# Optimization experiments

Measured on AMD Instinct MI355X. Metric: run time of the kernel, lower is better.

## Reference

```python
import jax, jax.numpy as jnp
import numpy as np

TAU = 2.0
V_TH = 1.0


def setup_inputs() -> dict:
    key = jax.random.key(0)
    k1, k2, k3 = jax.random.split(key, 3)
    T, B, N = 128, 64, 1024
    x = jax.random.normal(k1, (T, B, N), dtype=jnp.float32)
    # nn.Linear(hidden, hidden, bias=False) weights: [out, in]
    scale = 1.0 / np.sqrt(N)
    W1 = jax.random.uniform(k2, (N, N), dtype=jnp.float32, minval=-scale, maxval=scale)
    W2 = jax.random.uniform(k3, (N, N), dtype=jnp.float32, minval=-scale, maxval=scale)
    return {"x": x, "W1": W1, "W2": W2}


def _lif_scan(h_seq):
    # h_seq: [T, B, N]; LIF recurrence with tau=2, v_th=1, reset v = h*(1-s)
    def step(v, x_t):
        h = v + (x_t - v) / TAU
        s = (h >= V_TH).astype(h.dtype)
        return h * (1.0 - s), s

    v0 = jnp.zeros(h_seq.shape[1:], dtype=h_seq.dtype)
    _, spikes = jax.lax.scan(step, v0, h_seq)
    return spikes  # [T, B, N]


def reference(x, W1, W2):
    # fc1: y = x @ W1^T (torch Linear convention)
    h = jnp.einsum('tbn,mn->tbm', x, W1)
    spike = _lif_scan(h)
    return jnp.einsum('tbn,mn->tbm', spike, W2)
```

## Files before the change

### kernel.cpp

```cpp
#include <hip/hip_runtime.h>
#include <hip/hip_bf16.h>
#include <stdint.h>


#define TT 128
#define BB 64
#define NN 1024
#define MROWS (TT * BB)
#define SROW  (BB * NN)
#define MiB   ((size_t)1048576)

typedef _Float16 h8  __attribute__((ext_vector_type(8)));
typedef _Float16 h4v __attribute__((ext_vector_type(4)));
typedef float    f4  __attribute__((ext_vector_type(4)));
typedef float v2f __attribute__((ext_vector_type(2)));

#if __has_builtin(__builtin_elementwise_fma)
#define V2FMA(a, b, c) __builtin_elementwise_fma((a), (b), (c))
#else
static __device__ __forceinline__ v2f v2fma_(v2f a, v2f b, v2f c) {
    v2f r; r[0] = fmaf(a[0], b[0], c[0]); r[1] = fmaf(a[1], b[1], c[1]); return r;
}
#define V2FMA(a, b, c) v2fma_((a), (b), (c))
#endif

#define GL2LDS(g, l) __builtin_amdgcn_global_load_lds(                         \
    (const __attribute__((address_space(1))) void*)(const void*)(g),           \
    (__attribute__((address_space(3))) void*)(void*)(l), 16, 0, 0)

__global__ __launch_bounds__(256) void split2_f16(const float* __restrict__ src,
                                                  _Float16* __restrict__ d0,
                                                  _Float16* __restrict__ d1, int n4) {
    const int i = blockIdx.x * 256 + threadIdx.x;
    if (i >= n4) return;
    const float4 v = reinterpret_cast<const float4*>(src)[i];
    const float f[4] = {v.x, v.y, v.z, v.w};
    h4v a0, a1;
#pragma unroll
    for (int j = 0; j < 4; ++j) {
        const _Float16 c = (_Float16)f[j];
        a0[j] = c;
        a1[j] = (_Float16)((f[j] - (float)c) * 4096.0f);
    }
    reinterpret_cast<h4v*>(d0)[i] = a0;
    reinterpret_cast<h4v*>(d1)[i] = a1;
}

__global__ __launch_bounds__(256, 2) void gemm_split(const _Float16* __restrict__ A0,
                                                     const _Float16* __restrict__ A1,
                                                     const _Float16* __restrict__ B0,
                                                     const _Float16* __restrict__ B1,
                                                     float* __restrict__ C) {
    __shared__ _Float16 As[128 * 32];
    __shared__ _Float16 Bs[128 * 32];
    const int tid  = threadIdx.x;
    const int lane = tid & 63;
    const int wid  = tid >> 6;
    const int wr   = wid >> 1, wc = wid & 1;
    const int rowBase = blockIdx.y * 128;
    const int colBase = blockIdx.x * 128;

    const size_t aOff0 = (size_t)(rowBase + wid * 32 + (lane >> 2)) * NN + (lane & 3) * 8;
    const size_t aOff1 = aOff0 + (size_t)16 * NN;
    const size_t bOff0 = (size_t)(colBase + wid * 32 + (lane >> 2)) * NN + (lane & 3) * 8;
    const size_t bOff1 = bOff0 + (size_t)16 * NN;
    const int ldsW0 = (wid * 2 + 0) * 512;
    const int ldsW1 = (wid * 2 + 1) * 512;

    const int fA = (wr * 64 + (lane & 15)) * 32 + (lane >> 4) * 8;
    const int fB = (wc * 64 + (lane & 15)) * 32 + (lane >> 4) * 8;

    f4 acc0[4][4], acc1[4][4];
#pragma unroll
    for (int i = 0; i < 4; ++i)
#pragma unroll
        for (int j = 0; j < 4; ++j) { acc0[i][j] = (f4)0.0f; acc1[i][j] = (f4)0.0f; }

#define STAGE(AG, BG, K0)                                 \
    do {                                                  \
        GL2LDS((AG) + aOff0 + (K0), &As[ldsW0]);          \
        GL2LDS((AG) + aOff1 + (K0), &As[ldsW1]);          \
        GL2LDS((BG) + bOff0 + (K0), &Bs[ldsW0]);          \
        GL2LDS((BG) + bOff1 + (K0), &Bs[ldsW1]);          \
    } while (0)

#define PASS(AG, BG, ACC)                                                          \
    for (int k0 = 0; k0 < NN; k0 += 32) {                                          \
        STAGE(AG, BG, k0);                                                         \
        __syncthreads();                                                           \
        {                                                                          \
            h8 af0 = *(const h8*)&As[fA];                                          \
            h8 af1 = *(const h8*)&As[fA + 512];                                    \
            h8 af2 = *(const h8*)&As[fA + 1024];                                   \
            h8 af3 = *(const h8*)&As[fA + 1536];                                   \
            h8 bf0 = *(const h8*)&Bs[fB];                                          \
            h8 bf1 = *(const h8*)&Bs[fB + 512];                                    \
            h8 bf2 = *(const h8*)&Bs[fB + 1024];                                   \
            h8 bf3 = *(const h8*)&Bs[fB + 1536];                                   \
            ACC[0][0] = __builtin_amdgcn_mfma_f32_16x16x32_f16(af0, bf0, ACC[0][0], 0, 0, 0); \
            ACC[0][1] = __builtin_amdgcn_mfma_f32_16x16x32_f16(af0, bf1, ACC[0][1], 0, 0, 0); \
            ACC[0][2] = __builtin_amdgcn_mfma_f32_16x16x32_f16(af0, bf2, ACC[0][2], 0, 0, 0); \
            ACC[0][3] = __builtin_amdgcn_mfma_f32_16x16x32_f16(af0, bf3, ACC[0][3], 0, 0, 0); \
            ACC[1][0] = __builtin_amdgcn_mfma_f32_16x16x32_f16(af1, bf0, ACC[1][0], 0, 0, 0); \
            ACC[1][1] = __builtin_amdgcn_mfma_f32_16x16x32_f16(af1, bf1, ACC[1][1], 0, 0, 0); \
            ACC[1][2] = __builtin_amdgcn_mfma_f32_16x16x32_f16(af1, bf2, ACC[1][2], 0, 0, 0); \
            ACC[1][3] = __builtin_amdgcn_mfma_f32_16x16x32_f16(af1, bf3, ACC[1][3], 0, 0, 0); \
            ACC[2][0] = __builtin_amdgcn_mfma_f32_16x16x32_f16(af2, bf0, ACC[2][0], 0, 0, 0); \
            ACC[2][1] = __builtin_amdgcn_mfma_f32_16x16x32_f16(af2, bf1, ACC[2][1], 0, 0, 0); \
            ACC[2][2] = __builtin_amdgcn_mfma_f32_16x16x32_f16(af2, bf2, ACC[2][2], 0, 0, 0); \
            ACC[2][3] = __builtin_amdgcn_mfma_f32_16x16x32_f16(af2, bf3, ACC[2][3], 0, 0, 0); \
            ACC[3][0] = __builtin_amdgcn_mfma_f32_16x16x32_f16(af3, bf0, ACC[3][0], 0, 0, 0); \
            ACC[3][1] = __builtin_amdgcn_mfma_f32_16x16x32_f16(af3, bf1, ACC[3][1], 0, 0, 0); \
            ACC[3][2] = __builtin_amdgcn_mfma_f32_16x16x32_f16(af3, bf2, ACC[3][2], 0, 0, 0); \
            ACC[3][3] = __builtin_amdgcn_mfma_f32_16x16x32_f16(af3, bf3, ACC[3][3], 0, 0, 0); \
        }                                                                          \
        __syncthreads();                                                           \
    }

    PASS(A0, B0, acc0)
    PASS(A0, B1, acc1)
    PASS(A1, B0, acc1)
#undef PASS
#undef STAGE

    const int orow = rowBase + wr * 64 + (lane >> 4) * 4;
    const int ocol = colBase + wc * 64 + (lane & 15);
#pragma unroll
    for (int i = 0; i < 4; ++i)
#pragma unroll
        for (int j = 0; j < 4; ++j)
#pragma unroll
            for (int q = 0; q < 4; ++q)
                C[(size_t)(orow + i * 16 + q) * NN + ocol + j * 16] =
                    acc0[i][j][q] + acc1[i][j][q] * (1.0f / 4096.0f);
}

__global__ __launch_bounds__(256) void lif_scan(const float* __restrict__ H,
                                                unsigned long long* __restrict__ mask) {
    const int g = blockIdx.x * 256 + threadIdx.x;
    const int b = g >> 10;
    const int n = g & 1023;
    const int word = n >> 6;
    const bool lane0 = (threadIdx.x & 63) == 0;

    float v = 0.0f;
    float buf[8];
#pragma unroll
    for (int j = 0; j < 8; ++j) buf[j] = H[(size_t)j * SROW + g];

    for (int t0 = 0; t0 < TT; t0 += 8) {
        float nbuf[8];
        if (t0 + 8 < TT) {
#pragma unroll
            for (int j = 0; j < 8; ++j) nbuf[j] = H[(size_t)(t0 + 8 + j) * SROW + g];
        } else {
#pragma unroll
            for (int j = 0; j < 8; ++j) nbuf[j] = 0.f;
        }
#pragma unroll
        for (int j = 0; j < 8; ++j) {
            const float x = buf[j];
            const float h = v + (x - v) * 0.5f;
            const bool s = (h >= 1.0f);
            v = s ? 0.0f : h;
            const unsigned long long m = __ballot(s);
            if (lane0) mask[((size_t)(t0 + j) * BB + b) * 16 + word] = m;
        }
#pragma unroll
        for (int j = 0; j < 8; ++j) buf[j] = nbuf[j];
    }
}

__global__ __launch_bounds__(256) void transpose_nn(const float* __restrict__ in,
                                                    float* __restrict__ out) {
    __shared__ float tile[32][33];
    const int bx = blockIdx.x * 32, by = blockIdx.y * 32;
    {
        const int x = bx + threadIdx.x;
#pragma unroll
        for (int j = 0; j < 32; j += 8)
            tile[threadIdx.y + j][threadIdx.x] = in[(size_t)(by + threadIdx.y + j) * NN + x];
    }
    __syncthreads();
    {
        const int x = by + threadIdx.x;
#pragma unroll
        for (int j = 0; j < 32; j += 8)
            out[(size_t)(bx + threadIdx.y + j) * NN + x] = tile[threadIdx.x][threadIdx.y + j];
    }
}

__global__ __launch_bounds__(256) void spike_matmul(const unsigned long long* __restrict__ mask,
                                                    const float* __restrict__ W2T,
                                                    float* __restrict__ out) {
    __shared__ unsigned long long sw[16];
    const int r = blockIdx.x;
    const int tid = threadIdx.x;
    if (tid < 16) sw[tid] = mask[(size_t)r * 16 + tid];
    __syncthreads();

    float acc0 = 0.f, acc1 = 0.f, acc2 = 0.f, acc3 = 0.f;
#pragma unroll 1
    for (int w = 0; w < 16; ++w) {
        unsigned long long bits = sw[w];
        while (bits) {
            const int n = w * 64 + (__ffsll(bits) - 1);
            bits &= bits - 1;
            const float* __restrict__ row = W2T + (size_t)n * NN;
            acc0 += row[tid];
            acc1 += row[tid + 256];
            acc2 += row[tid + 512];
            acc3 += row[tid + 768];
        }
    }
    float* o = out + (size_t)r * NN;
    o[tid]       = acc0;
    o[tid + 256] = acc1;
    o[tid + 512] = acc2;
    o[tid + 768] = acc3;
}

#define BM 128
#define BN 64
#define BK 16
__global__ __launch_bounds__(256, 4) void gemm1_f32(const float* __restrict__ A,
                                                    const float* __restrict__ B,
                                                    float* __restrict__ C) {
    __shared__ float Asb[2][BK][132];
    __shared__ float Bsb[2][BK][68];
    const int tid = threadIdx.x;
    const int ty = tid >> 4;
    const int tx = tid & 15;
    const int rowBase = blockIdx.y * BM;
    const int colBase = blockIdx.x * BN;
    const int sr = tid >> 2;
    const int sk = (tid & 3) * 4;

    const float* Ap0 = A + (size_t)(rowBase + sr) * NN + sk;
    const float* Ap1 = Ap0 + (size_t)64 * NN;
    const float* Bp  = B + (size_t)(colBase + sr) * NN + sk;

    v2f acc[4][4];
#pragma unroll
    for (int i = 0; i < 4; ++i)
#pragma unroll
        for (int j = 0; j < 4; ++j) acc[i][j] = (v2f){0.f, 0.f};

    float4 ra0 = *(const float4*)Ap0;
    float4 ra1 = *(const float4*)Ap1;
    float4 rb  = *(const float4*)Bp;

#define STW(buf)                                                                       \
    do {                                                                               \
        Asb[buf][sk + 0][sr] = ra0.x; Asb[buf][sk + 1][sr] = ra0.y;                    \
        Asb[buf][sk + 2][sr] = ra0.z; Asb[buf][sk + 3][sr] = ra0.w;                    \
        Asb[buf][sk + 0][sr + 64] = ra1.x; Asb[buf][sk + 1][sr + 64] = ra1.y;          \
        Asb[buf][sk + 2][sr + 64] = ra1.z; Asb[buf][sk + 3][sr + 64] = ra1.w;          \
        Bsb[buf][sk + 0][sr] = rb.x;  Bsb[buf][sk + 1][sr] = rb.y;                     \
        Bsb[buf][sk + 2][sr] = rb.z;  Bsb[buf][sk + 3][sr] = rb.w;                     \
    } while (0)

    STW(0);
    __syncthreads();
    const int NT = NN / BK;
    for (int t = 0; t < NT; ++t) {
        const int cur = t & 1;
        if (t < NT - 1) {
            const int ko = (t + 1) * BK;
            ra0 = *(const float4*)(Ap0 + ko);
            ra1 = *(const float4*)(Ap1 + ko);
            rb  = *(const float4*)(Bp + ko);
        }
#pragma unroll
        for (int k = 0; k < BK; ++k) {
            const v2f* ap = (const v2f*)&Asb[cur][k][ty * 8];
            const float4 bf = *(const float4*)&Bsb[cur][k][tx * 4];
            const float bb[4] = {bf.x, bf.y, bf.z, bf.w};
            const v2f a0 = ap[0], a1 = ap[1], a2 = ap[2], a3 = ap[3];
#pragma unroll
            for (int j = 0; j < 4; ++j) {
                const v2f bd = {bb[j], bb[j]};
                acc[0][j] = V2FMA(a0, bd, acc[0][j]);
                acc[1][j] = V2FMA(a1, bd, acc[1][j]);
                acc[2][j] = V2FMA(a2, bd, acc[2][j]);
                acc[3][j] = V2FMA(a3, bd, acc[3][j]);
            }
        }
        if (t < NT - 1) STW(cur ^ 1);
        __syncthreads();
    }
#undef STW
    float* Cp = C + (size_t)(rowBase + ty * 8) * NN + colBase + tx * 4;
#pragma unroll
    for (int rp = 0; rp < 4; ++rp) {
        float4 lo = {acc[rp][0][0], acc[rp][1][0], acc[rp][2][0], acc[rp][3][0]};
        float4 hi = {acc[rp][0][1], acc[rp][1][1], acc[rp][2][1], acc[rp][3][1]};
        *(float4*)(Cp + (size_t)(2 * rp) * NN)     = lo;
        *(float4*)(Cp + (size_t)(2 * rp + 1) * NN) = hi;
    }
}

extern "C" void kernel_launch(void* const* d_in, const int* in_sizes, int n_in,
                              void* d_out, int out_size, void* d_ws, size_t ws_size,
                              hipStream_t stream) {
    const float* x  = (const float*)d_in[0];
    const float* W1 = (const float*)d_in[1];
    const float* W2 = (const float*)d_in[2];
    float* out = (float*)d_out;

    unsigned long long* mask = (unsigned long long*)d_ws;
    float* W2T = (float*)((char*)d_ws + 1 * MiB);

    if (ws_size >= 43 * MiB) {
        _Float16* A0 = (_Float16*)((char*)d_ws + 5 * MiB);
        _Float16* A1 = (_Float16*)((char*)d_ws + 22 * MiB);
        _Float16* B0 = (_Float16*)((char*)d_ws + 39 * MiB);
        _Float16* B1 = (_Float16*)((char*)d_ws + 41 * MiB);

        split2_f16<<<8192, 256, 0, stream>>>(x, A0, A1, MROWS * NN / 4);
        split2_f16<<<1024, 256, 0, stream>>>(W1, B0, B1, NN * NN / 4);
        transpose_nn<<<dim3(32, 32), dim3(32, 8), 0, stream>>>(W2, W2T);
        gemm_split<<<dim3(NN / 128, MROWS / 128), 256, 0, stream>>>(A0, A1, B0, B1, out);
    } else {
        transpose_nn<<<dim3(32, 32), dim3(32, 8), 0, stream>>>(W2, W2T);
        gemm1_f32<<<dim3(NN / BN, MROWS / BM), 256, 0, stream>>>(x, W1, out);
    }
    lif_scan<<<SROW / 256, 256, 0, stream>>>(out, mask);
    spike_matmul<<<MROWS, 256, 0, stream>>>(mask, W2T, out);
}
```

Before: 192.0 us.

## Double-buffer fused split GEMM, swizzle LDS, merge prep kernels, vectorize spike matmul

The three split-precision GEMM passes become a single K loop that loads all four fp16 operand tiles together, with a double-buffered LDS prefetch of the next K slice and XOR-swizzled LDS layout to cut bank conflicts. The two split kernels and the W2 transpose are merged into one prep launch to reduce launch overhead. The spike matmul now reads each W2T row as float4 vectors per thread instead of four strided scalars. LDS use per block quadruples (64 KiB), which may limit occupancy to fewer blocks per CU.

```diff
diff --git a/kernel.cpp b/kernel.cpp
--- a/kernel.cpp
+++ b/kernel.cpp
@@ -13,7 +13,7 @@
 typedef _Float16 h8  __attribute__((ext_vector_type(8)));
 typedef _Float16 h4v __attribute__((ext_vector_type(4)));
 typedef float    f4  __attribute__((ext_vector_type(4)));
-typedef float v2f __attribute__((ext_vector_type(2)));
+typedef float    v2f __attribute__((ext_vector_type(2)));
 
 #if __has_builtin(__builtin_elementwise_fma)
 #define V2FMA(a, b, c) __builtin_elementwise_fma((a), (b), (c))
@@ -28,22 +28,44 @@
     (const __attribute__((address_space(1))) void*)(const void*)(g),           \
     (__attribute__((address_space(3))) void*)(void*)(l), 16, 0, 0)
 
-__global__ __launch_bounds__(256) void split2_f16(const float* __restrict__ src,
-                                                  _Float16* __restrict__ d0,
-                                                  _Float16* __restrict__ d1, int n4) {
-    const int i = blockIdx.x * 256 + threadIdx.x;
-    if (i >= n4) return;
-    const float4 v = reinterpret_cast<const float4*>(src)[i];
-    const float f[4] = {v.x, v.y, v.z, v.w};
-    h4v a0, a1;
-#pragma unroll
-    for (int j = 0; j < 4; ++j) {
-        const _Float16 c = (_Float16)f[j];
-        a0[j] = c;
-        a1[j] = (_Float16)((f[j] - (float)c) * 4096.0f);
-    }
-    reinterpret_cast<h4v*>(d0)[i] = a0;
-    reinterpret_cast<h4v*>(d1)[i] = a1;
+__global__ __launch_bounds__(256) void prep(const float* __restrict__ x,
+                                            const float* __restrict__ W1,
+                                            const float* __restrict__ W2,
+                                            _Float16* __restrict__ A0, _Float16* __restrict__ A1,
+                                            _Float16* __restrict__ B0, _Float16* __restrict__ B1,
+                                            float* __restrict__ W2T) {
+    const int nb = blockIdx.x;
+    const int tid = threadIdx.x;
+    if (nb < 8192 + 1024) {
+        const bool isX = nb < 8192;
+        const float* src = isX ? x : W1;
+        _Float16* d0 = isX ? A0 : B0;
+        _Float16* d1 = isX ? A1 : B1;
+        const int i = (isX ? nb : nb - 8192) * 256 + tid;
+        const float4 v = reinterpret_cast<const float4*>(src)[i];
+        const float f[4] = {v.x, v.y, v.z, v.w};
+        h4v a0, a1;
+#pragma unroll
+        for (int j = 0; j < 4; ++j) {
+            const _Float16 c = (_Float16)f[j];
+            a0[j] = c;
+            a1[j] = (_Float16)((f[j] - (float)c) * 4096.0f);
+        }
+        reinterpret_cast<h4v*>(d0)[i] = a0;
+        reinterpret_cast<h4v*>(d1)[i] = a1;
+    } else {
+        __shared__ float tile[32][33];
+        const int tIdx = nb - 9216;
+        const int bx = (tIdx & 31) * 32, by = (tIdx >> 5) * 32;
+        const int tx = tid & 31, ty = tid >> 5;
+#pragma unroll
+        for (int j = 0; j < 32; j += 8)
+            tile[ty + j][tx] = W2[(size_t)(by + ty + j) * NN + bx + tx];
+        __syncthreads();
+#pragma unroll
+        for (int j = 0; j < 32; j += 8)
+            W2T[(size_t)(bx + ty + j) * NN + by + tx] = tile[tx][ty + j];
+    }
 }
 
 __global__ __launch_bounds__(256, 2) void gemm_split(const _Float16* __restrict__ A0,
@@ -51,8 +73,7 @@
                                                      const _Float16* __restrict__ B0,
                                                      const _Float16* __restrict__ B1,
                                                      float* __restrict__ C) {
-    __shared__ _Float16 As[128 * 32];
-    __shared__ _Float16 Bs[128 * 32];
+    __shared__ _Float16 As0[2][4096], As1[2][4096], Bs0[2][4096], Bs1[2][4096];
     const int tid  = threadIdx.x;
     const int lane = tid & 63;
     const int wid  = tid >> 6;
@@ -60,15 +81,23 @@
     const int rowBase = blockIdx.y * 128;
     const int colBase = blockIdx.x * 128;
 
-    const size_t aOff0 = (size_t)(rowBase + wid * 32 + (lane >> 2)) * NN + (lane & 3) * 8;
+    const int srow = wid * 32 + (lane >> 2);
+    const int swz  = (((lane & 3) ^ ((srow >> 1) & 3)) << 3);
+    const size_t aOff0 = (size_t)(rowBase + srow) * NN + swz;
     const size_t aOff1 = aOff0 + (size_t)16 * NN;
-    const size_t bOff0 = (size_t)(colBase + wid * 32 + (lane >> 2)) * NN + (lane & 3) * 8;
+    const size_t bOff0 = (size_t)(colBase + srow) * NN + swz;
     const size_t bOff1 = bOff0 + (size_t)16 * NN;
-    const int ldsW0 = (wid * 2 + 0) * 512;
-    const int ldsW1 = (wid * 2 + 1) * 512;
-
-    const int fA = (wr * 64 + (lane & 15)) * 32 + (lane >> 4) * 8;
-    const int fB = (wc * 64 + (lane & 15)) * 32 + (lane >> 4) * 8;
+    const int ldsB0 = wid * 1024;
+    const int ldsB1 = wid * 1024 + 512;
+
+    int fA[4], fB[4];
+#pragma unroll
+    for (int i = 0; i < 4; ++i) {
+        const int ra = wr * 64 + i * 16 + (lane & 15);
+        const int rb = wc * 64 + i * 16 + (lane & 15);
+        fA[i] = ra * 32 + (((lane >> 4) ^ ((ra >> 1) & 3)) << 3);
+        fB[i] = rb * 32 + (((lane >> 4) ^ ((rb >> 1) & 3)) << 3);
+    }
 
     f4 acc0[4][4], acc1[4][4];
 #pragma unroll
@@ -76,51 +105,43 @@
 #pragma unroll
         for (int j = 0; j < 4; ++j) { acc0[i][j] = (f4)0.0f; acc1[i][j] = (f4)0.0f; }
 
-#define STAGE(AG, BG, K0)                                 \
+#define STAGE(bi, K0)                                     \
     do {                                                  \
-        GL2LDS((AG) + aOff0 + (K0), &As[ldsW0]);          \
-        GL2LDS((AG) + aOff1 + (K0), &As[ldsW1]);          \
-        GL2LDS((BG) + bOff0 + (K0), &Bs[ldsW0]);          \
-        GL2LDS((BG) + bOff1 + (K0), &Bs[ldsW1]);          \
+        GL2LDS(A0 + aOff0 + (K0), &As0[bi][ldsB0]);       \
+        GL2LDS(A0 + aOff1 + (K0), &As0[bi][ldsB1]);       \
+        GL2LDS(A1 + aOff0 + (K0), &As1[bi][ldsB0]);       \
+        GL2LDS(A1 + aOff1 + (K0), &As1[bi][ldsB1]);       \
+        GL2LDS(B0 + bOff0 + (K0), &Bs0[bi][ldsB0]);       \
+        GL2LDS(B0 + bOff1 + (K0), &Bs0[bi][ldsB1]);       \
+        GL2LDS(B1 + bOff0 + (K0), &Bs1[bi][ldsB0]);       \
+        GL2LDS(B1 + bOff1 + (K0), &Bs1[bi][ldsB1]);       \
     } while (0)
 
-#define PASS(AG, BG, ACC)                                                          \
-    for (int k0 = 0; k0 < NN; k0 += 32) {                                          \
-        STAGE(AG, BG, k0);                                                         \
-        __syncthreads();                                                           \
-        {                                                                          \
-            h8 af0 = *(const h8*)&As[fA];                                          \
-            h8 af1 = *(const h8*)&As[fA + 512];                                    \
-            h8 af2 = *(const h8*)&As[fA + 1024];                                   \
-            h8 af3 = *(const h8*)&As[fA + 1536];                                   \
-            h8 bf0 = *(const h8*)&Bs[fB];                                          \
-            h8 bf1 = *(const h8*)&Bs[fB + 512];                                    \
-            h8 bf2 = *(const h8*)&Bs[fB + 1024];                                   \
-            h8 bf3 = *(const h8*)&Bs[fB + 1536];                                   \
-            ACC[0][0] = __builtin_amdgcn_mfma_f32_16x16x32_f16(af0, bf0, ACC[0][0], 0, 0, 0); \
-            ACC[0][1] = __builtin_amdgcn_mfma_f32_16x16x32_f16(af0, bf1, ACC[0][1], 0, 0, 0); \
-            ACC[0][2] = __builtin_amdgcn_mfma_f32_16x16x32_f16(af0, bf2, ACC[0][2], 0, 0, 0); \
-            ACC[0][3] = __builtin_amdgcn_mfma_f32_16x16x32_f16(af0, bf3, ACC[0][3], 0, 0, 0); \
-            ACC[1][0] = __builtin_amdgcn_mfma_f32_16x16x32_f16(af1, bf0, ACC[1][0], 0, 0, 0); \
-            ACC[1][1] = __builtin_amdgcn_mfma_f32_16x16x32_f16(af1, bf1, ACC[1][1], 0, 0, 0); \
-            ACC[1][2] = __builtin_amdgcn_mfma_f32_16x16x32_f16(af1, bf2, ACC[1][2], 0, 0, 0); \
-            ACC[1][3] = __builtin_amdgcn_mfma_f32_16x16x32_f16(af1, bf3, ACC[1][3], 0, 0, 0); \
-            ACC[2][0] = __builtin_amdgcn_mfma_f32_16x16x32_f16(af2, bf0, ACC[2][0], 0, 0, 0); \
-            ACC[2][1] = __builtin_amdgcn_mfma_f32_16x16x32_f16(af2, bf1, ACC[2][1], 0, 0, 0); \
-            ACC[2][2] = __builtin_amdgcn_mfma_f32_16x16x32_f16(af2, bf2, ACC[2][2], 0, 0, 0); \
-            ACC[2][3] = __builtin_amdgcn_mfma_f32_16x16x32_f16(af2, bf3, ACC[2][3], 0, 0, 0); \
-            ACC[3][0] = __builtin_amdgcn_mfma_f32_16x16x32_f16(af3, bf0, ACC[3][0], 0, 0, 0); \
-            ACC[3][1] = __builtin_amdgcn_mfma_f32_16x16x32_f16(af3, bf1, ACC[3][1], 0, 0, 0); \
-            ACC[3][2] = __builtin_amdgcn_mfma_f32_16x16x32_f16(af3, bf2, ACC[3][2], 0, 0, 0); \
-            ACC[3][3] = __builtin_amdgcn_mfma_f32_16x16x32_f16(af3, bf3, ACC[3][3], 0, 0, 0); \
-        }                                                                          \
-        __syncthreads();                                                           \
-    }
-
-    PASS(A0, B0, acc0)
-    PASS(A0, B1, acc1)
-    PASS(A1, B0, acc1)
-#undef PASS
+    STAGE(0, 0);
+    __syncthreads();
+
+    const int NT = NN / 32;
+    for (int t = 0; t < NT; ++t) {
+        const int cur = t & 1;
+        if (t < NT - 1) STAGE(cur ^ 1, (t + 1) * 32);
+        h8 a0f[4], a1f[4], b0f[4], b1f[4];
+#pragma unroll
+        for (int i = 0; i < 4; ++i) {
+            a0f[i] = *(const h8*)&As0[cur][fA[i]];
+            a1f[i] = *(const h8*)&As1[cur][fA[i]];
+            b0f[i] = *(const h8*)&Bs0[cur][fB[i]];
+            b1f[i] = *(const h8*)&Bs1[cur][fB[i]];
+        }
+#pragma unroll
+        for (int i = 0; i < 4; ++i)
+#pragma unroll
+            for (int j = 0; j < 4; ++j) {
+                acc0[i][j] = __builtin_amdgcn_mfma_f32_16x16x32_f16(a0f[i], b0f[j], acc0[i][j], 0, 0, 0);
+                acc1[i][j] = __builtin_amdgcn_mfma_f32_16x16x32_f16(a0f[i], b1f[j], acc1[i][j], 0, 0, 0);
+                acc1[i][j] = __builtin_amdgcn_mfma_f32_16x16x32_f16(a1f[i], b0f[j], acc1[i][j], 0, 0, 0);
+            }
+        __syncthreads();
+    }
 #undef STAGE
 
     const int orow = rowBase + wr * 64 + (lane >> 4) * 4;
@@ -168,25 +189,6 @@
         }
 #pragma unroll
         for (int j = 0; j < 8; ++j) buf[j] = nbuf[j];
-    }
-}
-
-__global__ __launch_bounds__(256) void transpose_nn(const float* __restrict__ in,
-                                                    float* __restrict__ out) {
-    __shared__ float tile[32][33];
-    const int bx = blockIdx.x * 32, by = blockIdx.y * 32;
-    {
-        const int x = bx + threadIdx.x;
-#pragma unroll
-        for (int j = 0; j < 32; j += 8)
-            tile[threadIdx.y + j][threadIdx.x] = in[(size_t)(by + threadIdx.y + j) * NN + x];
-    }
-    __syncthreads();
-    {
-        const int x = by + threadIdx.x;
-#pragma unroll
-        for (int j = 0; j < 32; j += 8)
-            out[(size_t)(bx + threadIdx.y + j) * NN + x] = tile[threadIdx.x][threadIdx.y + j];
     }
 }
 
@@ -199,25 +201,32 @@
     if (tid < 16) sw[tid] = mask[(size_t)r * 16 + tid];
     __syncthreads();
 
-    float acc0 = 0.f, acc1 = 0.f, acc2 = 0.f, acc3 = 0.f;
+    f4 acc = (f4)0.0f;
 #pragma unroll 1
     for (int w = 0; w < 16; ++w) {
         unsigned long long bits = sw[w];
         while (bits) {
             const int n = w * 64 + (__ffsll(bits) - 1);
             bits &= bits - 1;
-            const float* __restrict__ row = W2T + (size_t)n * NN;
-            acc0 += row[tid];
-            acc1 += row[tid + 256];
-            acc2 += row[tid + 512];
-            acc3 += row[tid + 768];
-        }
-    }
-    float* o = out + (size_t)r * NN;
-    o[tid]       = acc0;
-    o[tid + 256] = acc1;
-    o[tid + 512] = acc2;
-    o[tid + 768] = acc3;
+            const f4 rv = reinterpret_cast<const f4*>(W2T + (size_t)n * NN)[tid];
+            acc[0] += rv[0]; acc[1] += rv[1]; acc[2] += rv[2]; acc[3] += rv[3];
+        }
+    }
+    reinterpret_cast<f4*>(out + (size_t)r * NN)[tid] = acc;
+}
+
+__global__ __launch_bounds__(256) void transpose_nn(const float* __restrict__ in,
+                                                    float* __restrict__ out) {
+    __shared__ float tile[32][33];
+    const int bx = blockIdx.x * 32, by = blockIdx.y * 32;
+    const int tx = threadIdx.x, ty = threadIdx.y;
+#pragma unroll
+    for (int j = 0; j < 32; j += 8)
+        tile[ty + j][tx] = in[(size_t)(by + ty + j) * NN + bx + tx];
+    __syncthreads();
+#pragma unroll
+    for (int j = 0; j < 32; j += 8)
+        out[(size_t)(bx + ty + j) * NN + by + tx] = tile[tx][ty + j];
 }
 
 #define BM 128
@@ -317,9 +326,7 @@
         _Float16* B0 = (_Float16*)((char*)d_ws + 39 * MiB);
         _Float16* B1 = (_Float16*)((char*)d_ws + 41 * MiB);
 
-        split2_f16<<<8192, 256, 0, stream>>>(x, A0, A1, MROWS * NN / 4);
-        split2_f16<<<1024, 256, 0, stream>>>(W1, B0, B1, NN * NN / 4);
-        transpose_nn<<<dim3(32, 32), dim3(32, 8), 0, stream>>>(W2, W2T);
+        prep<<<8192 + 1024 + 1024, 256, 0, stream>>>(x, W1, W2, A0, A1, B0, B1, W2T);
         gemm_split<<<dim3(NN / 128, MROWS / 128), 256, 0, stream>>>(A0, A1, B0, B1, out);
     } else {
         transpose_nn<<<dim3(32, 32), dim3(32, 8), 0, stream>>>(W2, W2T);
```

Measured after the change: 181.3 us. -5.6%, faster.
